# Optimization experiments

Hardware: AMD Instinct MI355X
Metric: run time of the kernel (lower is better)

Reference implementation:

```python
import jax, jax.numpy as jnp
import numpy as np

PATCH = 8
GROUPS = 32
EPS = 1e-5


def group_norm(x, gamma, beta):
    # x: [B, C, H, W]; GroupNorm over (C//G, H, W) per group per sample
    B, C, H, W = x.shape
    xr = x.reshape(B, GROUPS, C // GROUPS, H, W)
    mu = xr.mean(axis=(2, 3, 4), keepdims=True)
    var = xr.var(axis=(2, 3, 4), keepdims=True)
    xn = ((xr - mu) * jax.lax.rsqrt(var + EPS)).reshape(B, C, H, W)
    return xn * gamma[None, :, None, None] + beta[None, :, None, None]


def patchify(x, p):
    # [B, C, H, W] -> [(B h w), C, p*p]  (matches einops 'b c (h p1) (w p2) -> (b h w) c (p1 p2)')
    B, C, H, W = x.shape
    h, w = H // p, W // p
    return x.reshape(B, C, h, p, w, p).transpose(0, 2, 4, 1, 3, 5).reshape(B * h * w, C, p * p)


def setup_inputs() -> dict:
    key = jax.random.key(0)
    ks = jax.random.split(key, 4)
    B, C, H, W = 8, 256, 128, 128
    x_low = jax.random.normal(ks[0], (B, C, H, W), dtype=jnp.float32)
    x_high = jax.random.normal(ks[1], (B, C, H, W), dtype=jnp.float32)
    # 1x1 conv weights [out_c, in_c] (kernel size 1 squeezed), no bias
    Wq = jax.random.normal(ks[2], (C, C), dtype=jnp.float32) / np.sqrt(C)
    Wk = jax.random.normal(ks[3], (C, C), dtype=jnp.float32) / np.sqrt(C)
    gq = jnp.ones((C,), jnp.float32)
    bq = jnp.zeros((C,), jnp.float32)
    gk = jnp.ones((C,), jnp.float32)
    bk = jnp.zeros((C,), jnp.float32)
    return {"x_low": x_low, "x_high": x_high, "Wq": Wq, "gq": gq, "bq": bq,
            "Wk": Wk, "gk": gk, "bk": bk}


def reference(x_low, x_high, Wq, gq, bq, Wk, gk, bk):
    p = PATCH
    B, C, H, W = x_low.shape
    h, w = H // p, W // p
    # conv_q / conv_k: 1x1 conv (no bias) + GroupNorm(32)
    qf = group_norm(jnp.einsum('bchw,oc->bohw', x_low, Wq), gq, bq)
    kf = group_norm(jnp.einsum('bchw,oc->bohw', x_high, Wk), gk, bk)
    q = patchify(qf, p).transpose(0, 2, 1)   # [N, P2, C]
    k = patchify(kf, p)                      # [N, C, P2]
    scale = jnp.asarray(np.power(C, 0.5), jnp.float32)
    attn = jax.nn.softmax(jnp.einsum('npc,ncq->npq', q, k) / scale, axis=-1)  # [N, P2, P2]
    out = jnp.einsum('npq,nqc->npc', attn, k.transpose(0, 2, 1))  # [N, P2, C], v = k^T
    # '(b h w) c (p1 p2) -> b c (h p1) (w p2)'
    out = out.reshape(B, h, w, p, p, C).transpose(0, 5, 1, 3, 2, 4).reshape(B, C, H, W)
    return out + x_low
```

## Files before the change

kernel.cpp:

```cpp
#include <hip/hip_runtime.h>
#include <cstdint>
#include <cstddef>

#define B_N   8
#define C_N   256
#define H_N   128
#define W_N   128
#define S_N   16384
#define CS_N  4194304
#define NELEM 33554432
#define EPS_F 1e-5f

__global__ __launch_bounds__(256) void conv_gemm(
    const float* __restrict__ x_low, const float* __restrict__ x_high,
    const float* __restrict__ Wq, const float* __restrict__ Wk,
    float* __restrict__ qf, float* __restrict__ kf)
{
  const int tid = threadIdx.x;
  const int tx = tid & 15, ty = tid >> 4;
  const int s0 = blockIdx.x * 128;
  const int o0 = blockIdx.y * 128;
  const int tensor = blockIdx.z >> 3;
  const int b = blockIdx.z & 7;

  const float* __restrict__ X = tensor ? x_high : x_low;
  const float* __restrict__ Wm = tensor ? Wk : Wq;
  float* __restrict__ Y = tensor ? kf : qf;

  __shared__ float As[16][128];
  __shared__ float Bs[16][132];

  float acc[8][8];
#pragma unroll
  for (int i = 0; i < 8; ++i)
#pragma unroll
    for (int j = 0; j < 8; ++j) acc[i][j] = 0.0f;

  const size_t xbase = (size_t)b * CS_N;
  const int a_oo = tid >> 1;
  const int a_kk = (tid & 1) * 8;
  const int b_kk = tid >> 4;
  const int b_ss = (tid & 15) * 8;

  int hw;
  {
    const int sp = s0 + b_ss;
    if (tensor) {
      const int nl = sp >> 6;
      const int r  = (sp >> 3) & 7;
      hw = (((nl >> 4) << 3) + r) * W_N + ((nl & 15) << 3);
    } else {
      hw = sp;
    }
  }
  const size_t xoff = xbase + (size_t)hw;

  for (int k0 = 0; k0 < 256; k0 += 16) {
    __syncthreads();
    {
      const float* src = Wm + ((size_t)(o0 + a_oo) * 256 + k0 + a_kk);
      const float4 w0 = *reinterpret_cast<const float4*>(src);
      const float4 w1 = *reinterpret_cast<const float4*>(src + 4);
      As[a_kk + 0][a_oo] = w0.x; As[a_kk + 1][a_oo] = w0.y;
      As[a_kk + 2][a_oo] = w0.z; As[a_kk + 3][a_oo] = w0.w;
      As[a_kk + 4][a_oo] = w1.x; As[a_kk + 5][a_oo] = w1.y;
      As[a_kk + 6][a_oo] = w1.z; As[a_kk + 7][a_oo] = w1.w;
    }
    {
      const float* src = X + (xoff + (size_t)(k0 + b_kk) * S_N);
      const float4 x0 = *reinterpret_cast<const float4*>(src);
      const float4 x1 = *reinterpret_cast<const float4*>(src + 4);
      Bs[b_kk][b_ss + 0] = x0.x; Bs[b_kk][b_ss + 1] = x0.y;
      Bs[b_kk][b_ss + 2] = x0.z; Bs[b_kk][b_ss + 3] = x0.w;
      Bs[b_kk][b_ss + 4] = x1.x; Bs[b_kk][b_ss + 5] = x1.y;
      Bs[b_kk][b_ss + 6] = x1.z; Bs[b_kk][b_ss + 7] = x1.w;
    }
    __syncthreads();
#pragma unroll
    for (int kk = 0; kk < 16; ++kk) {
      const float4 a0 = *reinterpret_cast<const float4*>(&As[kk][ty * 8]);
      const float4 a1 = *reinterpret_cast<const float4*>(&As[kk][ty * 8 + 4]);
      const float4 b0 = *reinterpret_cast<const float4*>(&Bs[kk][tx * 4]);
      const float4 b1 = *reinterpret_cast<const float4*>(&Bs[kk][64 + tx * 4]);
      const float av[8] = {a0.x, a0.y, a0.z, a0.w, a1.x, a1.y, a1.z, a1.w};
      const float bv[8] = {b0.x, b0.y, b0.z, b0.w, b1.x, b1.y, b1.z, b1.w};
#pragma unroll
      for (int i = 0; i < 8; ++i)
#pragma unroll
        for (int j = 0; j < 8; ++j) acc[i][j] = fmaf(av[i], bv[j], acc[i][j]);
    }
  }

#pragma unroll
  for (int i = 0; i < 8; ++i) {
    float* row = Y + (xbase + (size_t)(o0 + ty * 8 + i) * S_N + s0);
    *reinterpret_cast<float4*>(row + tx * 4) =
        make_float4(acc[i][0], acc[i][1], acc[i][2], acc[i][3]);
    *reinterpret_cast<float4*>(row + 64 + tx * 4) =
        make_float4(acc[i][4], acc[i][5], acc[i][6], acc[i][7]);
  }
}

__global__ __launch_bounds__(256) void gn_stats(
    const float* __restrict__ qf, const float* __restrict__ kf,
    float2* __restrict__ stats)
{
  const int bid = blockIdx.x;
  const int tensor = bid >> 8;
  const int rem = bid & 255;
  const int b = rem >> 5;
  const int g = rem & 31;
  const float* __restrict__ base =
      (tensor ? kf : qf) + (size_t)b * CS_N + (size_t)g * 8 * S_N;
  const float4* __restrict__ base4 = reinterpret_cast<const float4*>(base);

  const int tid = threadIdx.x;
  float s1 = 0.0f, s2 = 0.0f;
  for (int i = tid; i < 32768; i += 256) {
    const float4 u = base4[i];
    s1 += u.x + u.y + u.z + u.w;
    s2 += u.x * u.x + u.y * u.y + u.z * u.z + u.w * u.w;
  }
#pragma unroll
  for (int off = 32; off > 0; off >>= 1) {
    s1 += __shfl_down(s1, off);
    s2 += __shfl_down(s2, off);
  }
  __shared__ float r1[4], r2[4];
  const int wave = tid >> 6;
  if ((tid & 63) == 0) { r1[wave] = s1; r2[wave] = s2; }
  __syncthreads();
  if (tid == 0) {
    const float S1 = r1[0] + r1[1] + r1[2] + r1[3];
    const float S2 = r2[0] + r2[1] + r2[2] + r2[3];
    const float mean = S1 * (1.0f / 131072.0f);
    const float var = S2 * (1.0f / 131072.0f) - mean * mean;
    stats[bid] = make_float2(mean, rsqrtf(var + EPS_F));
  }
}

__global__ __launch_bounds__(256) void attn_kernel(
    const float* __restrict__ x_low,
    const float* __restrict__ gq, const float* __restrict__ bq,
    const float* __restrict__ gk, const float* __restrict__ bk,
    const float* __restrict__ qf, const float* __restrict__ kf,
    const float2* __restrict__ stats, float* __restrict__ out)
{
  const int n = ((blockIdx.x & 7) << 8) | (blockIdx.x >> 3);
  const int b = n >> 8;
  const int nl = n & 255;
  const int h0 = (nl >> 4) << 3, w0 = (nl & 15) << 3;
  const int t = threadIdx.x;
  const int tx = t & 15, ty = t >> 4;
  const int p = t & 63;
  const int ci = t >> 6;

  __shared__ float q_ch[64][68];
  __shared__ float k_ch[64][68];
  __shared__ float s_mat[64][68];
  __shared__ float red[4][64];
  __shared__ float rowstat[2][64];

  const int lc = t >> 2;
  const int lp = (t & 3) << 4;

  const size_t kbase = (size_t)b * CS_N + ((size_t)nl << 6) + lp;
  const size_t pixoff =
      (size_t)b * CS_N + (size_t)(h0 + (p >> 3)) * W_N + (w0 + (p & 7));

  float accs[4][4];
#pragma unroll
  for (int i = 0; i < 4; ++i)
#pragma unroll
    for (int j = 0; j < 4; ++j) accs[i][j] = 0.0f;

  for (int chunk = 0; chunk < 4; ++chunk) {
    __syncthreads();
    {
      const int c = (chunk << 6) + lc;
      const float2 sk = stats[256 + (b << 5) + (c >> 3)];
      const float ksc = gk[c] * sk.y;
      const float ksh = bk[c] - sk.x * ksc;
      const float4* src = reinterpret_cast<const float4*>(kf + kbase + (size_t)c * S_N);
      const float4 v0 = src[0], v1 = src[1], v2 = src[2], v3 = src[3];
      float4* dst = reinterpret_cast<float4*>(&k_ch[lc][lp]);
      dst[0] = make_float4(fmaf(v0.x, ksc, ksh), fmaf(v0.y, ksc, ksh),
                           fmaf(v0.z, ksc, ksh), fmaf(v0.w, ksc, ksh));
      dst[1] = make_float4(fmaf(v1.x, ksc, ksh), fmaf(v1.y, ksc, ksh),
                           fmaf(v1.z, ksc, ksh), fmaf(v1.w, ksc, ksh));
      dst[2] = make_float4(fmaf(v2.x, ksc, ksh), fmaf(v2.y, ksc, ksh),
                           fmaf(v2.z, ksc, ksh), fmaf(v2.w, ksc, ksh));
      dst[3] = make_float4(fmaf(v3.x, ksc, ksh), fmaf(v3.y, ksc, ksh),
                           fmaf(v3.z, ksc, ksh), fmaf(v3.w, ksc, ksh));
    }
    for (int cl = ci; cl < 64; cl += 4) {
      const int c = (chunk << 6) + cl;
      const float2 sq = stats[(b << 5) + (c >> 3)];
      const float qsc = gq[c] * sq.y * 0.0625f;
      const float qsh = (bq[c] - sq.x * gq[c] * sq.y) * 0.0625f;
      q_ch[cl][p] = fmaf(qf[pixoff + (size_t)c * S_N], qsc, qsh);
    }
    __syncthreads();
#pragma unroll 4
    for (int c = 0; c < 64; ++c) {
      const float4 qv = *reinterpret_cast<const float4*>(&q_ch[c][ty * 4]);
      const float4 kv = *reinterpret_cast<const float4*>(&k_ch[c][tx * 4]);
      const float qa[4] = {qv.x, qv.y, qv.z, qv.w};
      const float ka[4] = {kv.x, kv.y, kv.z, kv.w};
#pragma unroll
      for (int i = 0; i < 4; ++i)
#pragma unroll
        for (int j = 0; j < 4; ++j) accs[i][j] = fmaf(qa[i], ka[j], accs[i][j]);
    }
  }
#pragma unroll
  for (int j = 0; j < 4; ++j)
    *reinterpret_cast<float4*>(&s_mat[tx * 4 + j][ty * 4]) =
        make_float4(accs[0][j], accs[1][j], accs[2][j], accs[3][j]);
  __syncthreads();

  {
    float m = -3.0e38f;
#pragma unroll
    for (int rr = 0; rr < 16; ++rr) m = fmaxf(m, s_mat[ci * 16 + rr][p]);
    red[ci][p] = m;
    __syncthreads();
    if (t < 64)
      rowstat[0][t] = fmaxf(fmaxf(red[0][t], red[1][t]), fmaxf(red[2][t], red[3][t]));
    __syncthreads();
    const float rm = rowstat[0][p];
    float sum = 0.0f;
#pragma unroll
    for (int rr = 0; rr < 16; ++rr) {
      const float e = __expf(s_mat[ci * 16 + rr][p] - rm);
      s_mat[ci * 16 + rr][p] = e;
      sum += e;
    }
    red[ci][p] = sum;
    __syncthreads();
    if (t < 64) rowstat[1][t] = red[0][t] + red[1][t] + red[2][t] + red[3][t];
    __syncthreads();
  }
  const float rinv = 1.0f / rowstat[1][p];

  for (int chunk = 0; chunk < 4; ++chunk) {
    __syncthreads();
    {
      const int c = (chunk << 6) + lc;
      const float2 sk = stats[256 + (b << 5) + (c >> 3)];
      const float ksc = gk[c] * sk.y;
      const float ksh = bk[c] - sk.x * ksc;
      const float4* src = reinterpret_cast<const float4*>(kf + kbase + (size_t)c * S_N);
      const float4 v0 = src[0], v1 = src[1], v2 = src[2], v3 = src[3];
      const float vals[16] = {v0.x, v0.y, v0.z, v0.w, v1.x, v1.y, v1.z, v1.w,
                              v2.x, v2.y, v2.z, v2.w, v3.x, v3.y, v3.z, v3.w};
#pragma unroll
      for (int u = 0; u < 16; ++u) k_ch[lp + u][lc] = fmaf(vals[u], ksc, ksh);
    }
    __syncthreads();
    float accp[4][4];
#pragma unroll
    for (int i = 0; i < 4; ++i)
#pragma unroll
      for (int j = 0; j < 4; ++j) accp[i][j] = 0.0f;
#pragma unroll 4
    for (int r = 0; r < 64; ++r) {
      const float4 pv = *reinterpret_cast<const float4*>(&s_mat[r][ty * 4]);
      const float4 kv = *reinterpret_cast<const float4*>(&k_ch[r][tx * 4]);
      const float pa[4] = {pv.x, pv.y, pv.z, pv.w};
      const float ka[4] = {kv.x, kv.y, kv.z, kv.w};
#pragma unroll
      for (int i = 0; i < 4; ++i)
#pragma unroll
        for (int j = 0; j < 4; ++j) accp[i][j] = fmaf(pa[i], ka[j], accp[i][j]);
    }
#pragma unroll
    for (int i = 0; i < 4; ++i)
      *reinterpret_cast<float4*>(&q_ch[ty * 4 + i][tx * 4]) =
          make_float4(accp[i][0], accp[i][1], accp[i][2], accp[i][3]);
    __syncthreads();
    for (int cl = ci; cl < 64; cl += 4) {
      const size_t a = pixoff + (size_t)((chunk << 6) + cl) * S_N;
      out[a] = fmaf(q_ch[p][cl], rinv, x_low[a]);
    }
  }
}

extern "C" void kernel_launch(void* const* d_in, const int* in_sizes, int n_in,
                              void* d_out, int out_size, void* d_ws, size_t ws_size,
                              hipStream_t stream)
{
  const float* x_low  = (const float*)d_in[0];
  const float* x_high = (const float*)d_in[1];
  const float* Wq     = (const float*)d_in[2];
  const float* gq     = (const float*)d_in[3];
  const float* bq     = (const float*)d_in[4];
  const float* bk_    = (const float*)d_in[7];
  const float* Wk     = (const float*)d_in[5];
  const float* gk     = (const float*)d_in[6];
  float* out = (float*)d_out;

  float* qf = out;
  float* kf = (float*)d_ws;
  float2* stats = (float2*)((char*)d_ws + (size_t)NELEM * 4);

  dim3 gconv(128, 2, 16);
  hipLaunchKernelGGL(conv_gemm, gconv, dim3(256), 0, stream,
                     x_low, x_high, Wq, Wk, qf, kf);
  hipLaunchKernelGGL(gn_stats, dim3(512), dim3(256), 0, stream, qf, kf, stats);
  hipLaunchKernelGGL(attn_kernel, dim3(2048), dim3(256), 0, stream,
                     x_low, gq, bq, gk, bk_, qf, kf, stats, out);
}
```

Measured before the change: 854.3 us.

## Replace FP32 SIMT conv GEMM with split-bf16 MFMA and prepacked weights

Rewrites the 1x1 conv GEMM to use bf16 MFMA 16x16x32 instructions. It emulates fp32 accuracy by splitting each operand into hi and lo bf16 parts and issuing three MFMAs per tile. A small prep kernel packs the weights into MFMA fragment layout in workspace. Activations are converted to hi/lo in swizzled, double-buffered LDS, with global loads for the next K tile issued before the MFMAs. This trades 3x matrix-core work plus conversion overhead for much higher throughput than FP32 FMA, at some precision risk relative to true fp32.

After: 694.2 us. -18.7%, faster.

```diff
diff --git a/kernel.cpp b/kernel.cpp
--- a/kernel.cpp
+++ b/kernel.cpp
@@ -11,94 +11,194 @@
 #define NELEM 33554432
 #define EPS_F 1e-5f
 
-__global__ __launch_bounds__(256) void conv_gemm(
+typedef __attribute__((ext_vector_type(8))) short short8;
+typedef __attribute__((ext_vector_type(4))) float f32x4;
+
+union PackB { uint32_t w[4]; uint4 u4; short8 s8; };
+
+__device__ __forceinline__ uint32_t bf16_rne(float x) {
+  const uint32_t u = __float_as_uint(x);
+  return (u + 0x7FFFu + ((u >> 16) & 1u)) >> 16;
+}
+__device__ __forceinline__ uint32_t splitpack(float x) {
+  const uint32_t hi = bf16_rne(x);
+  const float r = x - __uint_as_float(hi << 16);
+  const uint32_t lo = bf16_rne(r);
+  return (hi << 16) | lo;
+}
+__device__ __forceinline__ int swz(int s, int c) {
+  return (s * 64 + c) ^ (((s & 3) << 3) | (s & 4));
+}
+
+__global__ __launch_bounds__(256) void prep_w(
+    const float* __restrict__ Wq, const float* __restrict__ Wk,
+    uint4* __restrict__ wpk)
+{
+  const int gid = blockIdx.x * 256 + threadIdx.x;
+  const int lane = gid & 63;
+  const int f = gid >> 6;
+  const int hl = f & 1;
+  const int mf = (f >> 1) & 15;
+  const int kf = (f >> 5) & 7;
+  const int tensor = (f >> 8) & 1;
+  const float* __restrict__ Wsrc = tensor ? Wk : Wq;
+
+  const int o  = mf * 16 + (lane & 15);
+  const int c0 = kf * 32 + ((lane >> 4) << 3);
+  const float* src = Wsrc + (size_t)o * 256 + c0;
+  const float4 x0 = *reinterpret_cast<const float4*>(src);
+  const float4 x1 = *reinterpret_cast<const float4*>(src + 4);
+  const float xs[8] = {x0.x, x0.y, x0.z, x0.w, x1.x, x1.y, x1.z, x1.w};
+
+  uint32_t h[8];
+#pragma unroll
+  for (int e = 0; e < 8; ++e) {
+    const uint32_t hi = bf16_rne(xs[e]);
+    if (hl == 0) {
+      h[e] = hi;
+    } else {
+      h[e] = bf16_rne(xs[e] - __uint_as_float(hi << 16));
+    }
+  }
+  uint4 outw;
+  outw.x = h[0] | (h[1] << 16);
+  outw.y = h[2] | (h[3] << 16);
+  outw.z = h[4] | (h[5] << 16);
+  outw.w = h[6] | (h[7] << 16);
+  wpk[(size_t)f * 64 + lane] = outw;
+}
+
+__global__ __launch_bounds__(256) void conv_mfma(
     const float* __restrict__ x_low, const float* __restrict__ x_high,
-    const float* __restrict__ Wq, const float* __restrict__ Wk,
+    const uint4* __restrict__ wpk,
     float* __restrict__ qf, float* __restrict__ kf)
 {
-  const int tid = threadIdx.x;
-  const int tx = tid & 15, ty = tid >> 4;
-  const int s0 = blockIdx.x * 128;
-  const int o0 = blockIdx.y * 128;
-  const int tensor = blockIdx.z >> 3;
-  const int b = blockIdx.z & 7;
+  const int t = threadIdx.x;
+  const int lane = t & 63;
+  const int w = t >> 6;
+  const int tile = blockIdx.x;
+  const int bz = blockIdx.y;
+  const int tensor = bz >> 3;
+  const int b = bz & 7;
 
   const float* __restrict__ X = tensor ? x_high : x_low;
-  const float* __restrict__ Wm = tensor ? Wk : Wq;
   float* __restrict__ Y = tensor ? kf : qf;
-
-  __shared__ float As[16][128];
-  __shared__ float Bs[16][132];
-
-  float acc[8][8];
-#pragma unroll
-  for (int i = 0; i < 8; ++i)
-#pragma unroll
-    for (int j = 0; j < 8; ++j) acc[i][j] = 0.0f;
+  const short8* __restrict__ wpkS = reinterpret_cast<const short8*>(wpk);
 
   const size_t xbase = (size_t)b * CS_N;
-  const int a_oo = tid >> 1;
-  const int a_kk = (tid & 1) * 8;
-  const int b_kk = tid >> 4;
-  const int b_ss = (tid & 15) * 8;
-
-  int hw;
+  const int s0 = tile * 64;
+
+  __shared__ uint32_t xb[2][4096];
+
+  const int cl = t >> 2;
+  const int sq = t & 3;
+  int offA, offB;
+  if (tensor) {
+    const int rA = 2 * sq, rB = 2 * sq + 1;
+    const int pb = ((tile >> 4) << 3) * W_N + ((tile & 15) << 3);
+    offA = pb + rA * W_N;
+    offB = pb + rB * W_N;
+  } else {
+    offA = s0 + sq * 16;
+    offB = offA + 8;
+  }
+  const float* __restrict__ Xb = X + xbase;
+
+  f32x4 acc[4][4] = {};
+
+  auto stage_write = [&](const float4& A0, const float4& A1,
+                         const float4& B0, const float4& B1, int nb) {
+    const float v[16] = {A0.x, A0.y, A0.z, A0.w, A1.x, A1.y, A1.z, A1.w,
+                         B0.x, B0.y, B0.z, B0.w, B1.x, B1.y, B1.z, B1.w};
+#pragma unroll
+    for (int jj = 0; jj < 16; ++jj) {
+      const int sl = sq * 16 + jj;
+      xb[nb][swz(sl, cl)] = splitpack(v[jj]);
+    }
+  };
+
   {
-    const int sp = s0 + b_ss;
-    if (tensor) {
-      const int nl = sp >> 6;
-      const int r  = (sp >> 3) & 7;
-      hw = (((nl >> 4) << 3) + r) * W_N + ((nl & 15) << 3);
-    } else {
-      hw = sp;
-    }
-  }
-  const size_t xoff = xbase + (size_t)hw;
-
-  for (int k0 = 0; k0 < 256; k0 += 16) {
-    __syncthreads();
-    {
-      const float* src = Wm + ((size_t)(o0 + a_oo) * 256 + k0 + a_kk);
-      const float4 w0 = *reinterpret_cast<const float4*>(src);
-      const float4 w1 = *reinterpret_cast<const float4*>(src + 4);
-      As[a_kk + 0][a_oo] = w0.x; As[a_kk + 1][a_oo] = w0.y;
-      As[a_kk + 2][a_oo] = w0.z; As[a_kk + 3][a_oo] = w0.w;
-      As[a_kk + 4][a_oo] = w1.x; As[a_kk + 5][a_oo] = w1.y;
-      As[a_kk + 6][a_oo] = w1.z; As[a_kk + 7][a_oo] = w1.w;
-    }
-    {
-      const float* src = X + (xoff + (size_t)(k0 + b_kk) * S_N);
-      const float4 x0 = *reinterpret_cast<const float4*>(src);
-      const float4 x1 = *reinterpret_cast<const float4*>(src + 4);
-      Bs[b_kk][b_ss + 0] = x0.x; Bs[b_kk][b_ss + 1] = x0.y;
-      Bs[b_kk][b_ss + 2] = x0.z; Bs[b_kk][b_ss + 3] = x0.w;
-      Bs[b_kk][b_ss + 4] = x1.x; Bs[b_kk][b_ss + 5] = x1.y;
-      Bs[b_kk][b_ss + 6] = x1.z; Bs[b_kk][b_ss + 7] = x1.w;
-    }
-    __syncthreads();
-#pragma unroll
-    for (int kk = 0; kk < 16; ++kk) {
-      const float4 a0 = *reinterpret_cast<const float4*>(&As[kk][ty * 8]);
-      const float4 a1 = *reinterpret_cast<const float4*>(&As[kk][ty * 8 + 4]);
-      const float4 b0 = *reinterpret_cast<const float4*>(&Bs[kk][tx * 4]);
-      const float4 b1 = *reinterpret_cast<const float4*>(&Bs[kk][64 + tx * 4]);
-      const float av[8] = {a0.x, a0.y, a0.z, a0.w, a1.x, a1.y, a1.z, a1.w};
-      const float bv[8] = {b0.x, b0.y, b0.z, b0.w, b1.x, b1.y, b1.z, b1.w};
-#pragma unroll
-      for (int i = 0; i < 8; ++i)
-#pragma unroll
-        for (int j = 0; j < 8; ++j) acc[i][j] = fmaf(av[i], bv[j], acc[i][j]);
-    }
-  }
-
-#pragma unroll
-  for (int i = 0; i < 8; ++i) {
-    float* row = Y + (xbase + (size_t)(o0 + ty * 8 + i) * S_N + s0);
-    *reinterpret_cast<float4*>(row + tx * 4) =
-        make_float4(acc[i][0], acc[i][1], acc[i][2], acc[i][3]);
-    *reinterpret_cast<float4*>(row + 64 + tx * 4) =
-        make_float4(acc[i][4], acc[i][5], acc[i][6], acc[i][7]);
-  }
+    const float* p = Xb + (size_t)cl * S_N;
+    const float4 A0 = *reinterpret_cast<const float4*>(p + offA);
+    const float4 A1 = *reinterpret_cast<const float4*>(p + offA + 4);
+    const float4 B0 = *reinterpret_cast<const float4*>(p + offB);
+    const float4 B1 = *reinterpret_cast<const float4*>(p + offB + 4);
+    stage_write(A0, A1, B0, B1, 0);
+  }
+
+  for (int kt = 0; kt < 4; ++kt) {
+    const int cur = kt & 1;
+    __syncthreads();
+
+    float4 nA0, nA1, nB0, nB1;
+    if (kt < 3) {
+      const float* p = Xb + (size_t)((kt + 1) * 64 + cl) * S_N;
+      nA0 = *reinterpret_cast<const float4*>(p + offA);
+      nA1 = *reinterpret_cast<const float4*>(p + offA + 4);
+      nB0 = *reinterpret_cast<const float4*>(p + offB);
+      nB1 = *reinterpret_cast<const float4*>(p + offB + 4);
+    }
+
+#pragma unroll
+    for (int ks = 0; ks < 2; ++ks) {
+      const int kfrag = kt * 2 + ks;
+      const int fbase = ((tensor * 8 + kfrag) * 16 + w * 4) * 2;
+      short8 a_hi[4], a_lo[4];
+#pragma unroll
+      for (int mf = 0; mf < 4; ++mf) {
+        a_hi[mf] = wpkS[(size_t)(fbase + mf * 2) * 64 + lane];
+        a_lo[mf] = wpkS[(size_t)(fbase + mf * 2 + 1) * 64 + lane];
+      }
+      short8 b_hi[4], b_lo[4];
+      const int c0 = ks * 32 + ((lane >> 4) << 3);
+#pragma unroll
+      for (int nf = 0; nf < 4; ++nf) {
+        const int sl = nf * 16 + (lane & 15);
+        const int wx = ((sl & 3) << 3) | (sl & 4);
+        const int base1 = ((sl * 64 + c0) ^ wx);
+        const int base2 = ((sl * 64 + c0 + 4) ^ wx);
+        const uint4 u = *reinterpret_cast<const uint4*>(&xb[cur][base1]);
+        const uint4 v = *reinterpret_cast<const uint4*>(&xb[cur][base2]);
+        PackB ph, pl;
+        ph.w[0] = __builtin_amdgcn_perm(u.y, u.x, 0x07060302u);
+        ph.w[1] = __builtin_amdgcn_perm(u.w, u.z, 0x07060302u);
+        ph.w[2] = __builtin_amdgcn_perm(v.y, v.x, 0x07060302u);
+        ph.w[3] = __builtin_amdgcn_perm(v.w, v.z, 0x07060302u);
+        pl.w[0] = __builtin_amdgcn_perm(u.y, u.x, 0x05040100u);
+        pl.w[1] = __builtin_amdgcn_perm(u.w, u.z, 0x05040100u);
+        pl.w[2] = __builtin_amdgcn_perm(v.y, v.x, 0x05040100u);
+        pl.w[3] = __builtin_amdgcn_perm(v.w, v.z, 0x05040100u);
+        b_hi[nf] = ph.s8;
+        b_lo[nf] = pl.s8;
+      }
+#pragma unroll
+      for (int mf = 0; mf < 4; ++mf)
+#pragma unroll
+        for (int nf = 0; nf < 4; ++nf) {
+          acc[mf][nf] = __builtin_amdgcn_mfma_f32_16x16x32_bf16(
+              a_hi[mf], b_hi[nf], acc[mf][nf], 0, 0, 0);
+          acc[mf][nf] = __builtin_amdgcn_mfma_f32_16x16x32_bf16(
+              a_hi[mf], b_lo[nf], acc[mf][nf], 0, 0, 0);
+          acc[mf][nf] = __builtin_amdgcn_mfma_f32_16x16x32_bf16(
+              a_lo[mf], b_hi[nf], acc[mf][nf], 0, 0, 0);
+        }
+    }
+
+    if (kt < 3) stage_write(nA0, nA1, nB0, nB1, cur ^ 1);
+  }
+
+  const int orow = w * 64 + ((lane >> 4) << 2);
+  const int scol = s0 + (lane & 15);
+#pragma unroll
+  for (int mf = 0; mf < 4; ++mf)
+#pragma unroll
+    for (int nf = 0; nf < 4; ++nf) {
+      const int o = orow + mf * 16;
+      const int s = scol + nf * 16;
+#pragma unroll
+      for (int r = 0; r < 4; ++r)
+        Y[xbase + (size_t)(o + r) * S_N + s] = acc[mf][nf][r];
+    }
 }
 
 __global__ __launch_bounds__(256) void gn_stats(
@@ -295,19 +395,20 @@
   const float* Wq     = (const float*)d_in[2];
   const float* gq     = (const float*)d_in[3];
   const float* bq     = (const float*)d_in[4];
-  const float* bk_    = (const float*)d_in[7];
   const float* Wk     = (const float*)d_in[5];
   const float* gk     = (const float*)d_in[6];
+  const float* bk     = (const float*)d_in[7];
   float* out = (float*)d_out;
 
   float* qf = out;
   float* kf = (float*)d_ws;
   float2* stats = (float2*)((char*)d_ws + (size_t)NELEM * 4);
-
-  dim3 gconv(128, 2, 16);
-  hipLaunchKernelGGL(conv_gemm, gconv, dim3(256), 0, stream,
-                     x_low, x_high, Wq, Wk, qf, kf);
+  uint4* wpk = (uint4*)((char*)d_ws + (size_t)NELEM * 4 + 4096);
+
+  hipLaunchKernelGGL(prep_w, dim3(128), dim3(256), 0, stream, Wq, Wk, wpk);
+  hipLaunchKernelGGL(conv_mfma, dim3(256, 16), dim3(256), 0, stream,
+                     x_low, x_high, wpk, qf, kf);
   hipLaunchKernelGGL(gn_stats, dim3(512), dim3(256), 0, stream, qf, kf, stats);
   hipLaunchKernelGGL(attn_kernel, dim3(2048), dim3(256), 0, stream,
-                     x_low, gq, bq, gk, bk_, qf, kf, stats, out);
-}
+                     x_low, gq, bq, gk, bk, qf, kf, stats, out);
+}
```
